# Kernel tuning notes

Hardware: AMD Instinct MI355X
Metric: run time of the kernel (lower is better)

Reference implementation:

```python
import jax, jax.numpy as jnp
import numpy as np

KERNEL_SIZE = 9

def setup_inputs() -> dict:
    key = jax.random.key(0)
    k1, k2 = jax.random.split(key)
    x = jax.random.normal(k1, (32, 16384, 8), dtype=jnp.float32)
    W = jax.random.normal(k2, (8, KERNEL_SIZE), dtype=jnp.float32) * 0.05  # 'random_normal' init
    b = jnp.zeros((1,), dtype=jnp.float32)
    return {"x": x, "W": W, "b": b}

def reference(x, W, b):
    # x: (B, S, F); W: (F, K); b: (1,)
    K = W.shape[1]
    S = x.shape[1]
    new_steps = S - K  # matches original: steps - kernel_size
    base = x[:, :new_steps, :] * W[:, 0]          # (B, N, F)
    peaks = jnp.zeros_like(base)
    # loop over small fixed kernel (K-1 = 8 iterations), vectorized over B, N, F
    for k in range(K - 1):
        shifted = x[:, k:k + new_steps, :] * W[:, k + 1]  # (B, N, F)
        peaks = peaks + jnp.abs(base - shifted)
    return peaks + b  # bias (1,) broadcasts over features, as in original
```

## Files before the change

### kernel.cpp

```cpp
#include <hip/hip_runtime.h>

#define B_DIM 32
#define S_DIM 16384
#define F_DIM 8
#define K_DIM 9
#define N_DIM (S_DIM - K_DIM)

__global__ __launch_bounds__(256) void peak2peak_kernel(
    const float* __restrict__ x,
    const float* __restrict__ W,
    const float* __restrict__ bias,
    float* __restrict__ out)
{
    int tid = blockIdx.x * blockDim.x + threadIdx.x;
    const int total = B_DIM * N_DIM;
    if (tid >= total) return;

    int b = tid / N_DIM;
    int n = tid - b * N_DIM;

    const float* xrow = x + ((long)b * S_DIM + (long)n) * F_DIM;

    float w0[F_DIM];
#pragma unroll
    for (int f = 0; f < F_DIM; ++f) w0[f] = W[f * K_DIM + 0];

    float4 b0 = *reinterpret_cast<const float4*>(xrow);
    float4 b1 = *reinterpret_cast<const float4*>(xrow + 4);
    float base[F_DIM] = {
        b0.x * w0[0], b0.y * w0[1], b0.z * w0[2], b0.w * w0[3],
        b1.x * w0[4], b1.y * w0[5], b1.z * w0[6], b1.w * w0[7]
    };

    float acc[F_DIM] = {0.f, 0.f, 0.f, 0.f, 0.f, 0.f, 0.f, 0.f};

#pragma unroll
    for (int k = 0; k < K_DIM - 1; ++k) {
        float4 r0 = *reinterpret_cast<const float4*>(xrow + (long)k * F_DIM);
        float4 r1 = *reinterpret_cast<const float4*>(xrow + (long)k * F_DIM + 4);
        float rr[F_DIM] = { r0.x, r0.y, r0.z, r0.w, r1.x, r1.y, r1.z, r1.w };
#pragma unroll
        for (int f = 0; f < F_DIM; ++f) {
            acc[f] += fabsf(base[f] - rr[f] * W[f * K_DIM + (k + 1)]);
        }
    }

    float bb = bias[0];
    float4 o0 = { acc[0] + bb, acc[1] + bb, acc[2] + bb, acc[3] + bb };
    float4 o1 = { acc[4] + bb, acc[5] + bb, acc[6] + bb, acc[7] + bb };

    float* orow = out + (long)tid * F_DIM;
    *reinterpret_cast<float4*>(orow) = o0;
    *reinterpret_cast<float4*>(orow + 4) = o1;
}

extern "C" void kernel_launch(void* const* d_in, const int* in_sizes, int n_in,
                              void* d_out, int out_size, void* d_ws, size_t ws_size,
                              hipStream_t stream) {
    const float* x    = (const float*)d_in[0];
    const float* W    = (const float*)d_in[1];
    const float* bias = (const float*)d_in[2];
    float* out        = (float*)d_out;

    const int total  = B_DIM * N_DIM;
    const int block  = 256;
    const int grid   = (total + block - 1) / block;

    peak2peak_kernel<<<grid, block, 0, stream>>>(x, W, bias, out);
}
```

Before: 12.70 us.

## Stage input windows in swizzled LDS tiles per batch-row block

Each block now handles 256 positions of one batch row and loads the 264-row halo window cooperatively into shared memory with an XOR swizzle, then reads the 8 shifted rows from LDS instead of issuing 8 overlapping global loads per thread. A 2D grid removes the per-thread division. This removes redundant global/L2 traffic for the overlapping windows, at the cost of a block-wide barrier and LDS bank-conflict handling.

```diff
diff --git a/kernel.cpp b/kernel.cpp
--- a/kernel.cpp
+++ b/kernel.cpp
@@ -1,10 +1,12 @@
 #include <hip/hip_runtime.h>
 
-#define B_DIM 32
-#define S_DIM 16384
-#define F_DIM 8
-#define K_DIM 9
-#define N_DIM (S_DIM - K_DIM)
+#define BATCH  32
+#define S_DIM  16384
+#define F_DIM  8
+#define K_DIM  9
+#define N_DIM  (S_DIM - K_DIM)
+#define NPB    256
+#define CHUNKS 528
 
 __global__ __launch_bounds__(256) void peak2peak_kernel(
     const float* __restrict__ x,
@@ -12,46 +14,66 @@
     const float* __restrict__ bias,
     float* __restrict__ out)
 {
-    int tid = blockIdx.x * blockDim.x + threadIdx.x;
-    const int total = B_DIM * N_DIM;
-    if (tid >= total) return;
+    __shared__ float4 lds4[CHUNKS];
 
-    int b = tid / N_DIM;
-    int n = tid - b * N_DIM;
+    const int t  = threadIdx.x;
+    const int b  = blockIdx.y;
+    const int n0 = blockIdx.x << 8;
 
-    const float* xrow = x + ((long)b * S_DIM + (long)n) * F_DIM;
-
-    float w0[F_DIM];
-#pragma unroll
-    for (int f = 0; f < F_DIM; ++f) w0[f] = W[f * K_DIM + 0];
-
-    float4 b0 = *reinterpret_cast<const float4*>(xrow);
-    float4 b1 = *reinterpret_cast<const float4*>(xrow + 4);
-    float base[F_DIM] = {
-        b0.x * w0[0], b0.y * w0[1], b0.z * w0[2], b0.w * w0[3],
-        b1.x * w0[4], b1.y * w0[5], b1.z * w0[6], b1.w * w0[7]
-    };
-
-    float acc[F_DIM] = {0.f, 0.f, 0.f, 0.f, 0.f, 0.f, 0.f, 0.f};
+    const float* xbase = x + ((long)b * S_DIM + n0) * F_DIM;
+    const int climit = 2 * (S_DIM - n0);
 
 #pragma unroll
-    for (int k = 0; k < K_DIM - 1; ++k) {
-        float4 r0 = *reinterpret_cast<const float4*>(xrow + (long)k * F_DIM);
-        float4 r1 = *reinterpret_cast<const float4*>(xrow + (long)k * F_DIM + 4);
-        float rr[F_DIM] = { r0.x, r0.y, r0.z, r0.w, r1.x, r1.y, r1.z, r1.w };
-#pragma unroll
-        for (int f = 0; f < F_DIM; ++f) {
-            acc[f] += fabsf(base[f] - rr[f] * W[f * K_DIM + (k + 1)]);
+    for (int i = 0; i < 3; ++i) {
+        int c = t + i * 256;
+        if (c < CHUNKS && c < climit) {
+            float4 v = *reinterpret_cast<const float4*>(xbase + c * 4);
+            *reinterpret_cast<float4*>(
+                reinterpret_cast<char*>(lds4) + ((c ^ ((c >> 3) & 7)) << 4)) = v;
         }
     }
+    __syncthreads();
 
-    float bb = bias[0];
-    float4 o0 = { acc[0] + bb, acc[1] + bb, acc[2] + bb, acc[3] + bb };
-    float4 o1 = { acc[4] + bb, acc[5] + bb, acc[6] + bb, acc[7] + bb };
+    const float bb = bias[0];
+    float res[F_DIM];
 
-    float* orow = out + (long)tid * F_DIM;
-    *reinterpret_cast<float4*>(orow) = o0;
-    *reinterpret_cast<float4*>(orow + 4) = o1;
+#pragma unroll
+    for (int j = 0; j < 2; ++j) {
+        float4 rv[8];
+#pragma unroll
+        for (int k = 0; k < 8; ++k) {
+            int row = t + k;
+            int byteoff = ((2 * row + j) ^ ((row >> 2) & 7)) << 4;
+            rv[k] = *reinterpret_cast<const float4*>(
+                reinterpret_cast<const char*>(lds4) + byteoff);
+        }
+        float rr0[4] = { rv[0].x, rv[0].y, rv[0].z, rv[0].w };
+        float basev[4], acc[4];
+#pragma unroll
+        for (int f = 0; f < 4; ++f) {
+            basev[f] = rr0[f] * W[(4 * j + f) * K_DIM];
+            acc[f]   = 0.f;
+        }
+#pragma unroll
+        for (int k = 0; k < 8; ++k) {
+            float rr[4] = { rv[k].x, rv[k].y, rv[k].z, rv[k].w };
+#pragma unroll
+            for (int f = 0; f < 4; ++f) {
+                acc[f] += fabsf(basev[f] - rr[f] * W[(4 * j + f) * K_DIM + k + 1]);
+            }
+        }
+#pragma unroll
+        for (int f = 0; f < 4; ++f) res[4 * j + f] = acc[f] + bb;
+    }
+
+    const int n = n0 + t;
+    if (n < N_DIM) {
+        float* orow = out + ((long)b * N_DIM + n) * F_DIM;
+        float4 o0 = { res[0], res[1], res[2], res[3] };
+        float4 o1 = { res[4], res[5], res[6], res[7] };
+        *reinterpret_cast<float4*>(orow)     = o0;
+        *reinterpret_cast<float4*>(orow + 4) = o1;
+    }
 }
 
 extern "C" void kernel_launch(void* const* d_in, const int* in_sizes, int n_in,
@@ -62,9 +84,6 @@
     const float* bias = (const float*)d_in[2];
     float* out        = (float*)d_out;
 
-    const int total  = B_DIM * N_DIM;
-    const int block  = 256;
-    const int grid   = (total + block - 1) / block;
-
-    peak2peak_kernel<<<grid, block, 0, stream>>>(x, W, bias, out);
+    dim3 grid(S_DIM / NPB, BATCH);
+    peak2peak_kernel<<<grid, 256, 0, stream>>>(x, W, bias, out);
 }
```

Result: no change. 12.62 us (median of 2 runs) (-0.6%).
